# Performance work log

Hardware: AMD Instinct MI355X
Metric: run time of the kernel (lower is better)

The kernel has to match this reference:

```python
import jax, jax.numpy as jnp
import numpy as np
from jax import lax

B, N_ENT, D_ENT = 64, 512, 256
C_SCAT, C_MAP, W = 32, 18, 64
N_RES = 4


def conv2d(x, w, stride, pad):
    return lax.conv_general_dilated(x, w, (stride, stride), [(pad, pad), (pad, pad)],
                                    dimension_numbers=('NCHW', 'OIHW', 'NCHW'))


def batchnorm(x, g, b, eps=1e-5):
    # training-mode BN (batch statistics), matching nn.BatchNorm2d default train()
    mu = x.mean((0, 2, 3), keepdims=True)
    var = x.var((0, 2, 3), keepdims=True)
    return g[None, :, None, None] * (x - mu) * lax.rsqrt(var + eps) + b[None, :, None, None]


def setup_inputs() -> dict:
    key = jax.random.key(0)
    ks = jax.random.split(key, 24)
    s = 0.05
    inp = {
        'x': jax.random.uniform(ks[0], (B, C_MAP, W, W), jnp.float32),
        'entity_embeddings': jax.random.normal(ks[1], (B, N_ENT, D_ENT), jnp.float32),
        'entity_x_y': jax.random.randint(ks[2], (B, N_ENT, 16), 0, 2, jnp.int32),
        'conv1_w': jax.random.normal(ks[3], (C_SCAT, D_ENT), jnp.float32) * s,
        'project_w': jax.random.normal(ks[4], (32, C_SCAT + C_MAP, 1, 1), jnp.float32) * s,
        'project_b': jnp.zeros((32,), jnp.float32),
        'ds1_w': jax.random.normal(ks[5], (64, 32, 4, 4), jnp.float32) * s,
        'ds1_b': jnp.zeros((64,), jnp.float32),
        'ds2_w': jax.random.normal(ks[6], (128, 64, 4, 4), jnp.float32) * s,
        'ds2_b': jnp.zeros((128,), jnp.float32),
        'ds3_w': jax.random.normal(ks[7], (128, 128, 4, 4), jnp.float32) * s,
        'ds3_b': jnp.zeros((128,), jnp.float32),
        'res_conv1_w': jax.random.normal(ks[8], (N_RES, 128, 128, 3, 3), jnp.float32) * s,
        'res_bn1_g': jnp.ones((N_RES, 128), jnp.float32),
        'res_bn1_b': jnp.zeros((N_RES, 128), jnp.float32),
        'res_conv2_w': jax.random.normal(ks[9], (N_RES, 128, 128, 3, 3), jnp.float32) * s,
        'res_bn2_g': jnp.ones((N_RES, 128), jnp.float32),
        'res_bn2_b': jnp.zeros((N_RES, 128), jnp.float32),
        'fc_w': jax.random.normal(ks[10], (256, 8 * 8 * 128), jnp.float32) * s,
        'fc_b': jnp.zeros((256,), jnp.float32),
    }
    return inp


def _scatter(entity_embeddings, entity_x_y, conv1_w):
    # reduced = relu(Conv1d(256->32, k=1)) on entity dim
    reduced = jax.nn.relu(jnp.einsum('bnd,cd->bnc', entity_embeddings, conv1_w))  # [B,N,32]
    bits = entity_x_y
    pow2 = (2 ** jnp.arange(7, -1, -1)).astype(jnp.int32)
    xv = (bits[..., :8] * pow2).sum(-1) // 4   # [B,N] in 0..63
    yv = (bits[..., 8:] * pow2).sum(-1) // 4
    valid = (bits[..., 0] != -1000000000)
    reduced = reduced * valid[..., None].astype(reduced.dtype)
    b_idx = jnp.arange(entity_embeddings.shape[0], dtype=jnp.int32)[:, None]
    flat = (b_idx * (W * W) + yv * W + xv).reshape(-1)
    scat = jax.ops.segment_sum(reduced.reshape(-1, C_SCAT), flat, num_segments=entity_embeddings.shape[0] * W * W)
    return scat.reshape(-1, W, W, C_SCAT).transpose(0, 3, 1, 2)  # [B,32,W,W]


def reference(x, entity_embeddings, entity_x_y, conv1_w, project_w, project_b,
              ds1_w, ds1_b, ds2_w, ds2_b, ds3_w, ds3_b,
              res_conv1_w, res_bn1_g, res_bn1_b, res_conv2_w, res_bn2_g, res_bn2_b,
              fc_w, fc_b):
    scatter_map = _scatter(entity_embeddings, entity_x_y, conv1_w)
    h = jnp.concatenate([scatter_map, x], axis=1)  # [B,50,64,64]
    h = jax.nn.relu(conv2d(h, project_w, 1, 0) + project_b[None, :, None, None])
    h = jax.nn.relu(conv2d(h, ds1_w, 2, 1) + ds1_b[None, :, None, None])   # [B,64,32,32]
    h = jax.nn.relu(conv2d(h, ds2_w, 2, 1) + ds2_b[None, :, None, None])   # [B,128,16,16]
    h = jax.nn.relu(conv2d(h, ds3_w, 2, 1) + ds3_b[None, :, None, None])   # [B,128,8,8]
    map_skip = h
    for i in range(N_RES):
        identity = h
        o = batchnorm(conv2d(h, res_conv1_w[i], 1, 1), res_bn1_g[i], res_bn1_b[i])
        o = jax.nn.relu(o)
        o = batchnorm(conv2d(o, res_conv2_w[i], 1, 1), res_bn2_g[i], res_bn2_b[i])
        h = jax.nn.relu(o + identity)
        map_skip = map_skip + h
    flat = h.reshape(h.shape[0], -1)
    embedded_spatial = jax.nn.relu(flat @ fc_w.T + fc_b)
    return (map_skip, embedded_spatial)
```

## Files before the change

kernel.cpp:

```cpp
#include <hip/hip_runtime.h>
#include <hip/hip_bf16.h>

typedef __attribute__((ext_vector_type(8))) short bf16x8;
typedef __attribute__((ext_vector_type(4))) short bf16x4;
typedef __attribute__((ext_vector_type(4))) float f32x4;

__device__ __forceinline__ short f2bs(float v) {
  __hip_bfloat16 h = __float2bfloat16(v);
  return *reinterpret_cast<short*>(&h);
}

__global__ __launch_bounds__(256) void k_wall(
    const float* __restrict__ rc1w, const float* __restrict__ rc2w,
    const float* __restrict__ d1w, const float* __restrict__ d2w,
    const float* __restrict__ d3w, const float* __restrict__ fcw,
    const float* __restrict__ c1w, const float* __restrict__ pw,
    short* __restrict__ wTr1, short* __restrict__ wTr2, short* __restrict__ wTds1,
    short* __restrict__ wTds2, short* __restrict__ wTds3, short* __restrict__ wfcbf,
    short* __restrict__ wsc, short* __restrict__ wproj,
    float* __restrict__ scat, float* __restrict__ stats) {
  __shared__ float ld[128 * 65];
  const int bx = blockIdx.x;
  const int tid = threadIdx.x;
  if (bx < 8192) {
    ((float4*)scat)[(size_t)bx * 256 + tid] = make_float4(0.f, 0.f, 0.f, 0.f);
  } else if (bx < 12800) {
    const float* src = (bx < 10496) ? rc1w : rc2w;
    short* dst = (bx < 10496) ? wTr1 : wTr2;
    const int i = ((bx - 8192) % 2304) * 256 + tid;
    if (i < 589824) {
      const int layer = i / 147456;
      const int rem = i % 147456;
      const int tap = rem / 16384;
      const int r2 = rem & 16383;
      const int co = r2 >> 7, ci = r2 & 127;
      dst[i] = f2bs(src[(((size_t)layer * 16384 + co * 128 + ci) * 9) + tap]);
    }
  } else if (bx < 14464) {
    int n, base;
    const float* src;
    short* dst;
    if (bx < 12928) { n = 32768; base = 12800; src = d1w; dst = wTds1; }
    else if (bx < 13440) { n = 131072; base = 12928; src = d2w; dst = wTds2; }
    else { n = 262144; base = 13440; src = d3w; dst = wTds3; }
    const int i = (bx - base) * 256 + tid;
    if (i < n) {
      const int COCI = n / 16;
      const int tap = i / COCI;
      const int rem = i % COCI;
      dst[i] = f2bs(src[(size_t)rem * 16 + tap]);
    }
  } else if (bx < 14720) {
    const int j = bx - 14464;
    const float* sp = fcw + (size_t)j * 8192;
    for (int i = tid; i < 8192; i += 256) {
      const int co = i >> 6, pix = i & 63;
      ld[co * 65 + pix] = sp[i];
    }
    __syncthreads();
    short* dp = wfcbf + (size_t)j * 8192;
    for (int i = tid; i < 8192; i += 256) {
      const int pix = i >> 7, co = i & 127;
      dp[i] = f2bs(ld[co * 65 + pix]);
    }
  } else if (bx < 14752) {
    const int i = (bx - 14720) * 256 + tid;
    if (i < 8192) wsc[i] = f2bs(c1w[i]);
  } else if (bx < 14760) {
    const int i = (bx - 14752) * 256 + tid;
    if (i < 2048) {
      const int co = i >> 6, k = i & 63;
      wproj[i] = (k < 50) ? f2bs(pw[co * 50 + k]) : (short)0;
    }
  } else {
    for (int i = tid; i < 2048; i += 256) stats[i] = 0.f;
  }
}

__global__ __launch_bounds__(256) void k_scatmfma(const float* __restrict__ emb,
                                                  const int* __restrict__ xy,
                                                  const short* __restrict__ wsc,
                                                  float* __restrict__ scat_pm) {
  constexpr int CIP = 264;
  __shared__ short abf[64 * CIP];
  __shared__ int flat[64];
  const int tid = threadIdx.x;
  const int e0 = blockIdx.x * 64;
  const float4* eg = (const float4*)(emb + (size_t)e0 * 256);
  for (int i = tid; i < 4096; i += 256) {
    const int e = i >> 6, k4 = i & 63;
    const float4 v = eg[(size_t)e * 64 + k4];
    bf16x4 o;
    o[0] = f2bs(v.x); o[1] = f2bs(v.y); o[2] = f2bs(v.z); o[3] = f2bs(v.w);
    *(bf16x4*)(&abf[e * CIP + k4 * 4]) = o;
  }
  if (tid < 64) {
    const int* bp = xy + (size_t)(e0 + tid) * 16;
    int xv = 0, yv = 0;
#pragma unroll
    for (int j = 0; j < 8; ++j) xv = (xv << 1) | bp[j];
#pragma unroll
    for (int j = 8; j < 16; ++j) yv = (yv << 1) | bp[j];
    flat[tid] = (bp[0] != -1000000000)
                    ? (((e0 + tid) >> 9) * 4096 + ((yv >> 2) << 6) + (xv >> 2))
                    : -1;
  }
  __syncthreads();
  const int wq = __builtin_amdgcn_readfirstlane(tid >> 6);
  const int lane = tid & 63;
  const int l15 = lane & 15, quad = lane >> 4;
  f32x4 acc[2];
  acc[0] = (f32x4){0.f, 0.f, 0.f, 0.f};
  acc[1] = (f32x4){0.f, 0.f, 0.f, 0.f};
  const short* arow = &abf[(wq * 16 + l15) * CIP + quad * 8];
  const short* w0 = wsc + (size_t)l15 * 256 + quad * 8;
  const short* w1 = wsc + (size_t)(16 + l15) * 256 + quad * 8;
#pragma unroll
  for (int kk = 0; kk < 8; ++kk) {
    bf16x8 a = *(const bf16x8*)(arow + kk * 32);
    acc[0] = __builtin_amdgcn_mfma_f32_16x16x32_bf16(a, *(const bf16x8*)(w0 + kk * 32), acc[0], 0, 0, 0);
    acc[1] = __builtin_amdgcn_mfma_f32_16x16x32_bf16(a, *(const bf16x8*)(w1 + kk * 32), acc[1], 0, 0, 0);
  }
#pragma unroll
  for (int nt = 0; nt < 2; ++nt)
#pragma unroll
    for (int r = 0; r < 4; ++r) {
      const int e = wq * 16 + quad * 4 + r;
      const float v = acc[nt][r];
      const int f = flat[e];
      if (f >= 0 && v > 0.f)
        atomicAdd(&scat_pm[(size_t)f * 32 + nt * 16 + l15], v);
    }
}

__global__ __launch_bounds__(256) void k_projmfma(const float* __restrict__ scat_pm,
                                                  const float* __restrict__ xin,
                                                  const short* __restrict__ wproj,
                                                  const float* __restrict__ pb,
                                                  short* __restrict__ h0pm) {
  constexpr int PK = 72;
  __shared__ short abf[128 * PK];
  const int tid = threadIdx.x;
  const int b = blockIdx.x >> 5;
  const int yx0 = (blockIdx.x & 31) << 7;
  const float4* sg = (const float4*)(scat_pm + ((size_t)(b * 4096 + yx0)) * 32);
  for (int i = tid; i < 1024; i += 256) {
    const int p = i >> 3, c4 = i & 7;
    const float4 v = sg[(size_t)p * 8 + c4];
    bf16x4 o;
    o[0] = f2bs(v.x); o[1] = f2bs(v.y); o[2] = f2bs(v.z); o[3] = f2bs(v.w);
    *(bf16x4*)(&abf[p * PK + c4 * 4]) = o;
  }
  for (int i = tid; i < 2304; i += 256) {
    const int run = i >> 7, p = i & 127;
    abf[p * PK + 32 + run] = f2bs(xin[(size_t)(b * 18 + run) * 4096 + yx0 + p]);
  }
  for (int i = tid; i < 2048; i += 256) {
    const int p = i >> 4, k = 50 + (i & 15);
    abf[p * PK + k] = 0;
  }
  __syncthreads();
  const int wq = __builtin_amdgcn_readfirstlane(tid >> 6);
  const int lane = tid & 63;
  const int l15 = lane & 15, quad = lane >> 4;
  f32x4 acc[2][2];
#pragma unroll
  for (int t = 0; t < 2; ++t)
#pragma unroll
    for (int n = 0; n < 2; ++n) acc[t][n] = (f32x4){0.f, 0.f, 0.f, 0.f};
  const short* wb0 = wproj + (size_t)l15 * 64 + quad * 8;
  const short* wb1 = wproj + (size_t)(16 + l15) * 64 + quad * 8;
#pragma unroll
  for (int kk = 0; kk < 2; ++kk) {
    const bf16x8 b0 = *(const bf16x8*)(wb0 + kk * 32);
    const bf16x8 b1 = *(const bf16x8*)(wb1 + kk * 32);
#pragma unroll
    for (int t = 0; t < 2; ++t) {
      const int pix = (wq * 2 + t) * 16 + l15;
      bf16x8 a = *(const bf16x8*)(&abf[pix * PK + quad * 8 + kk * 32]);
      acc[t][0] = __builtin_amdgcn_mfma_f32_16x16x32_bf16(a, b0, acc[t][0], 0, 0, 0);
      acc[t][1] = __builtin_amdgcn_mfma_f32_16x16x32_bf16(a, b1, acc[t][1], 0, 0, 0);
    }
  }
#pragma unroll
  for (int t = 0; t < 2; ++t)
#pragma unroll
    for (int n = 0; n < 2; ++n) {
      const int co = n * 16 + l15;
      const float bv = pb[co];
#pragma unroll
      for (int r = 0; r < 4; ++r) {
        const int pix = (wq * 2 + t) * 16 + quad * 4 + r;
        float v = acc[t][n][r] + bv;
        v = v > 0.f ? v : 0.f;
        h0pm[((size_t)(b * 4096 + yx0 + pix)) * 32 + co] = f2bs(v);
      }
    }
}

template <int CIN, int COUT, int HIN, int ROWSO, int COSPLIT, int MT, int NT, int OUTMODE>
__global__ __launch_bounds__(256) void k_ds2(const short* __restrict__ inpm,
                                             const short* __restrict__ wT,
                                             const float* __restrict__ bias,
                                             short* __restrict__ outbf,
                                             float* __restrict__ outf,
                                             float* __restrict__ msf) {
  constexpr int HOUT = HIN / 2;
  constexpr int ROWS = 2 * ROWSO + 2;
  constexpr int COLS = HIN + 2;
  constexpr int CHUNKS = CIN / 8;
  constexpr int KK = CIN / 32;
  constexpr int CIPAD = CIN + 8;
  constexpr int NHO = HOUT / ROWSO;
  __shared__ short lin[ROWS * COLS * CIPAD];
  const int tid = threadIdx.x;
  int bx = blockIdx.x;
  const int co_blk = (COSPLIT > 1) ? (bx % COSPLIT) : 0;
  if (COSPLIT > 1) bx /= COSPLIT;
  const int hoblk = bx % NHO;
  const int b = bx / NHO;
  for (int i = tid; i < ROWS * COLS * CHUNKS; i += 256) {
    const int ch = i % CHUNKS;
    const int pixv = i / CHUNKS;
    const int r = pixv / COLS, c = pixv % COLS;
    const int hi = 2 * ROWSO * hoblk - 1 + r;
    const int wc = c - 1;
    bf16x8 v = (bf16x8)(short)0;
    if (hi >= 0 && hi < HIN && wc >= 0 && wc < HIN)
      v = *(const bf16x8*)(inpm + ((size_t)(b * HIN + hi) * HIN + wc) * CIN + ch * 8);
    *(bf16x8*)(&lin[(r * COLS + c) * CIPAD + ch * 8]) = v;
  }
  __syncthreads();
  const int wq = __builtin_amdgcn_readfirstlane(tid >> 6);
  const int lane = tid & 63;
  const int l15 = lane & 15, quad = lane >> 4;
  const int mtile = (MT > 1) ? (wq % MT) : 0;
  const int cogrp = wq / MT;
  const int cobase = co_blk * (COUT / COSPLIT) + cogrp * (NT * 16);
  const int p = mtile * 16 + l15;
  const int dr = p / HOUT;
  const int col = p % HOUT;
  f32x4 acc[NT];
#pragma unroll
  for (int n = 0; n < NT; ++n) acc[n] = (f32x4){0.f, 0.f, 0.f, 0.f};
  const short* wrow = wT + (size_t)(cobase + l15) * CIN + quad * 8;
  for (int ky = 0; ky < 4; ++ky) {
    for (int kx = 0; kx < 4; ++kx) {
      const short* arow = &lin[((2 * dr + ky) * COLS + 2 * col + kx) * CIPAD + quad * 8];
      const short* wt = wrow + (size_t)(ky * 4 + kx) * COUT * CIN;
#pragma unroll
      for (int kk = 0; kk < KK; ++kk) {
        bf16x8 a = *(const bf16x8*)(arow + kk * 32);
#pragma unroll
        for (int n = 0; n < NT; ++n) {
          bf16x8 bf = *(const bf16x8*)(wt + n * 16 * CIN + kk * 32);
          acc[n] = __builtin_amdgcn_mfma_f32_16x16x32_bf16(a, bf, acc[n], 0, 0, 0);
        }
      }
    }
  }
#pragma unroll
  for (int n = 0; n < NT; ++n) {
    const int co = cobase + n * 16 + l15;
    const float bv = bias[co];
#pragma unroll
    for (int r = 0; r < 4; ++r) {
      const int pp = mtile * 16 + quad * 4 + r;
      const int dr2 = pp / HOUT;
      const int c2 = pp % HOUT;
      const int ho = hoblk * ROWSO + dr2;
      float v = acc[n][r] + bv;
      v = v > 0.f ? v : 0.f;
      const size_t o = ((size_t)b * HOUT * HOUT + ho * HOUT + c2) * COUT + co;
      outbf[o] = f2bs(v);
      if (OUTMODE == 1) {
        outf[o] = v;
        msf[o] = v;
      }
    }
  }
}

template <int BNIN>
__global__ __launch_bounds__(256) void k_resmfma(const short* __restrict__ hbfin,
                                                 const float* __restrict__ fin,
                                                 const float* __restrict__ statsIn,
                                                 const float* __restrict__ gIn,
                                                 const float* __restrict__ bIn,
                                                 const float* __restrict__ identpm,
                                                 float* __restrict__ houtpm,
                                                 float* __restrict__ mspm,
                                                 const short* __restrict__ wT,
                                                 float* __restrict__ outpm,
                                                 float* __restrict__ statsOut) {
  constexpr int CIPAD = 136;
  __shared__ short lin[100 * CIPAD];
  __shared__ float bnsc[128], bnsh[128];
  const int tid = threadIdx.x;
  const int b = blockIdx.x >> 3;
  const int cobase = (blockIdx.x & 7) << 4;
  if (BNIN >= 1) {
    if (tid < 128) {
      const float mu = statsIn[tid] * (1.f / 4096.f);
      const float var = statsIn[128 + tid] * (1.f / 4096.f) - mu * mu;
      const float sc = gIn[tid] * rsqrtf(var + 1e-5f);
      bnsc[tid] = sc;
      bnsh[tid] = bIn[tid] - mu * sc;
    }
    __syncthreads();
  }
  if (BNIN == 0) {
    const short* hb = hbfin + ((size_t)b << 13);
    for (int i = tid; i < 1600; i += 256) {
      const int pixel = i >> 4, ch = i & 15;
      const int r = pixel / 10, c = pixel % 10;
      bf16x8 v = (bf16x8)(short)0;
      if (r >= 1 && r <= 8 && c >= 1 && c <= 8)
        v = *(const bf16x8*)(hb + (((r - 1) << 3) + (c - 1)) * 128 + ch * 8);
      *(bf16x8*)(&lin[pixel * CIPAD + ch * 8]) = v;
    }
  } else if (BNIN == 1) {
    const float* fb = fin + ((size_t)b << 13);
    for (int i = tid; i < 3200; i += 256) {
      const int pixel = i >> 5, c4 = i & 31;
      const int r = pixel / 10, c = pixel % 10;
      bf16x4 o = (bf16x4)(short)0;
      if (r >= 1 && r <= 8 && c >= 1 && c <= 8) {
        const float4 x = *(const float4*)(fb + (size_t)(((r - 1) << 3) + (c - 1)) * 128 + c4 * 4);
        const float xv[4] = {x.x, x.y, x.z, x.w};
#pragma unroll
        for (int k = 0; k < 4; ++k) {
          const int ci = c4 * 4 + k;
          const float v = xv[k] * bnsc[ci] + bnsh[ci];
          o[k] = f2bs(v > 0.f ? v : 0.f);
        }
      }
      *(bf16x4*)(&lin[pixel * CIPAD + c4 * 4]) = o;
    }
  } else {
    const float* fb = fin + ((size_t)b << 13);
    const float* ib = identpm + ((size_t)b << 13);
    float* hb = houtpm + ((size_t)b << 13);
    float* mb = mspm + ((size_t)b << 13);
    const bool wr = (cobase == 0);
    for (int i = tid; i < 3200; i += 256) {
      const int pixel = i >> 5, c4 = i & 31;
      const int r = pixel / 10, c = pixel % 10;
      bf16x4 o = (bf16x4)(short)0;
      if (r >= 1 && r <= 8 && c >= 1 && c <= 8) {
        const size_t gi = (size_t)(((r - 1) << 3) + (c - 1)) * 128 + c4 * 4;
        const float4 x = *(const float4*)(fb + gi);
        const float4 idv = *(const float4*)(ib + gi);
        const float xv[4] = {x.x, x.y, x.z, x.w};
        const float iv[4] = {idv.x, idv.y, idv.z, idv.w};
        float vv[4];
#pragma unroll
        for (int k = 0; k < 4; ++k) {
          const int ci = c4 * 4 + k;
          float v = xv[k] * bnsc[ci] + bnsh[ci] + iv[k];
          v = v > 0.f ? v : 0.f;
          vv[k] = v;
          o[k] = f2bs(v);
        }
        if (wr) {
          *(float4*)(hb + gi) = make_float4(vv[0], vv[1], vv[2], vv[3]);
          const float4 m = *(const float4*)(mb + gi);
          *(float4*)(mb + gi) = make_float4(m.x + vv[0], m.y + vv[1], m.z + vv[2], m.w + vv[3]);
        }
      }
      *(bf16x4*)(&lin[pixel * CIPAD + c4 * 4]) = o;
    }
  }
  __syncthreads();
  const int wq = __builtin_amdgcn_readfirstlane(tid >> 6);
  const int lane = tid & 63;
  const int l15 = lane & 15, quad = lane >> 4;
  const int p = wq * 16 + l15;
  const int py = p >> 3, px = p & 7;
  f32x4 acc = (f32x4){0.f, 0.f, 0.f, 0.f};
  const short* wrow = wT + (size_t)(cobase + l15) * 128 + quad * 8;
  for (int t = 0; t < 9; ++t) {
    const int ky = t / 3, kx = t % 3;
    const short* arow = &lin[((py + ky) * 10 + px + kx) * CIPAD + quad * 8];
    const short* wt = wrow + (size_t)t * 16384;
#pragma unroll
    for (int kk = 0; kk < 4; ++kk) {
      bf16x8 a = *(const bf16x8*)(arow + kk * 32);
      bf16x8 bf = *(const bf16x8*)(wt + kk * 32);
      acc = __builtin_amdgcn_mfma_f32_16x16x32_bf16(a, bf, acc, 0, 0, 0);
    }
  }
  float* ob = outpm + ((size_t)b << 13);
  const int co = cobase + l15;
  float s = 0.f, q = 0.f;
#pragma unroll
  for (int r = 0; r < 4; ++r) {
    const float v = acc[r];
    ob[(size_t)(wq * 16 + quad * 4 + r) * 128 + co] = v;
    s += v;
    q += v * v;
  }
  s += __shfl_down(s, 32); q += __shfl_down(q, 32);
  s += __shfl_down(s, 16); q += __shfl_down(q, 16);
  if (lane < 16) {
    atomicAdd(&statsOut[co], s);
    atomicAdd(&statsOut[128 + co], q);
  }
}

__global__ __launch_bounds__(256) void k_bnfinal(const float* __restrict__ tmp2pm,
                                                 const float* __restrict__ stats,
                                                 const float* __restrict__ g,
                                                 const float* __restrict__ bb,
                                                 const float* __restrict__ identpm,
                                                 const float* __restrict__ mspm,
                                                 float* __restrict__ out0,
                                                 short* __restrict__ hbf) {
  __shared__ float t[64 * 132];
  __shared__ float bnsc[128], bnsh[128];
  const int b = blockIdx.x;
  const int tid = threadIdx.x;
  if (tid < 128) {
    const float mu = stats[tid] * (1.f / 4096.f);
    const float var = stats[128 + tid] * (1.f / 4096.f) - mu * mu;
    const float sc = g[tid] * rsqrtf(var + 1e-5f);
    bnsc[tid] = sc;
    bnsh[tid] = bb[tid] - mu * sc;
  }
  __syncthreads();
  const size_t base = (size_t)b << 13;
  for (int i = tid; i < 8192; i += 256) {
    const int co = i & 127, pix = i >> 7;
    float v = tmp2pm[base + i] * bnsc[co] + bnsh[co] + identpm[base + i];
    v = v > 0.f ? v : 0.f;
    hbf[base + i] = f2bs(v);
    t[pix * 132 + co] = mspm[base + i] + v;
  }
  __syncthreads();
  float* dp = out0 + base;
  for (int i = tid; i < 8192; i += 256) {
    const int co = i >> 6, pix = i & 63;
    dp[i] = t[pix * 132 + co];
  }
}

__global__ __launch_bounds__(256) void k_fcmfma(const short* __restrict__ hbf,
                                                const short* __restrict__ wbf,
                                                float* __restrict__ part) {
  const int nb = blockIdx.x & 3;
  const int kb = blockIdx.x >> 2;
  const int wq = __builtin_amdgcn_readfirstlane((int)(threadIdx.x >> 6));
  const int lane = threadIdx.x & 63;
  const int l15 = lane & 15, quad = lane >> 4;
  const int k0 = kb * 256 + quad * 8;
  const short* wp = wbf + (size_t)(nb * 64 + wq * 16 + l15) * 8192 + k0;
  const short* hp = hbf + (size_t)l15 * 8192 + k0;
  f32x4 acc[4];
#pragma unroll
  for (int m = 0; m < 4; ++m) acc[m] = (f32x4){0.f, 0.f, 0.f, 0.f};
  for (int ks = 0; ks < 8; ++ks) {
    bf16x8 bfr = *(const bf16x8*)(wp + ks * 32);
#pragma unroll
    for (int m = 0; m < 4; ++m) {
      bf16x8 a = *(const bf16x8*)(hp + (size_t)m * 16 * 8192 + ks * 32);
      acc[m] = __builtin_amdgcn_mfma_f32_16x16x32_bf16(a, bfr, acc[m], 0, 0, 0);
    }
  }
#pragma unroll
  for (int m = 0; m < 4; ++m)
#pragma unroll
    for (int r = 0; r < 4; ++r) {
      const int b = m * 16 + quad * 4 + r;
      part[((size_t)kb * 64 + b) * 256 + nb * 64 + wq * 16 + l15] = acc[m][r];
    }
}

__global__ __launch_bounds__(256) void k_fcred(const float* __restrict__ part,
                                               const float* __restrict__ bias,
                                               float* __restrict__ out1) {
  const int idx = blockIdx.x * 256 + threadIdx.x;
  const int j = idx & 255;
  float s = 0.f;
#pragma unroll 8
  for (int kb = 0; kb < 32; ++kb) s += part[(size_t)kb * 16384 + idx];
  const float v = s + bias[j];
  out1[idx] = v > 0.f ? v : 0.f;
}

extern "C" void kernel_launch(void* const* d_in, const int* in_sizes, int n_in,
                              void* d_out, int out_size, void* d_ws, size_t ws_size,
                              hipStream_t stream) {
  const float* xin = (const float*)d_in[0];
  const float* emb = (const float*)d_in[1];
  const int* xy = (const int*)d_in[2];
  const float* c1w = (const float*)d_in[3];
  const float* pw = (const float*)d_in[4];
  const float* pb = (const float*)d_in[5];
  const float* d1w = (const float*)d_in[6];
  const float* d1b = (const float*)d_in[7];
  const float* d2w = (const float*)d_in[8];
  const float* d2b = (const float*)d_in[9];
  const float* d3w = (const float*)d_in[10];
  const float* d3b = (const float*)d_in[11];
  const float* rc1w = (const float*)d_in[12];
  const float* rbn1g = (const float*)d_in[13];
  const float* rbn1b = (const float*)d_in[14];
  const float* rc2w = (const float*)d_in[15];
  const float* rbn2g = (const float*)d_in[16];
  const float* rbn2b = (const float*)d_in[17];
  const float* fcw = (const float*)d_in[18];
  const float* fcb = (const float*)d_in[19];

  float* out0 = (float*)d_out;
  float* out1 = out0 + 524288;

  float* F = (float*)d_ws;
  float* scat = F + 0;
  float* h1pm_f = F + 0;
  float* h2pm_f = F + 2097152;
  float* hApm = F + 3145728;
  float* hBpm = F + 3670016;
  float* tmppm = F + 4194304;
  float* tmp2pm = F + 4718592;
  float* mspm = F + 5242880;
  short* pmbfA = (short*)(F + 5767168);
  short* hfinbf = (short*)(F + 6029312);
  float* stats = F + 6291456;
  float* fcpart = F + 6293504;
  short* h0pm = (short*)(F + 8388608);
  short* wfcbf = (short*)(F + 12582912);
  short* wTr1 = (short*)(F + 13631488);
  short* wTr2 = wTr1 + 589824;
  short* wTds1 = wTr2 + 589824;
  short* wTds2 = wTds1 + 32768;
  short* wTds3 = wTds2 + 131072;
  short* wsc = wTds3 + 262144;
  short* wproj = wsc + 8192;

  k_wall<<<14761, 256, 0, stream>>>(rc1w, rc2w, d1w, d2w, d3w, fcw, c1w, pw,
                                    wTr1, wTr2, wTds1, wTds2, wTds3, wfcbf, wsc, wproj,
                                    scat, stats);
  k_scatmfma<<<512, 256, 0, stream>>>(emb, xy, wsc, scat);
  k_projmfma<<<2048, 256, 0, stream>>>(scat, xin, wproj, pb, h0pm);
  short* h1pm = (short*)h1pm_f;
  short* h2pm = (short*)h2pm_f;
  k_ds2<32, 64, 64, 2, 1, 4, 4, 0><<<1024, 256, 0, stream>>>(h0pm, wTds1, d1b, h1pm, hApm, mspm);
  k_ds2<64, 128, 32, 1, 1, 1, 2, 0><<<1024, 256, 0, stream>>>(h1pm, wTds2, d2b, h2pm, hApm, mspm);
  k_ds2<128, 128, 16, 2, 2, 1, 1, 1><<<512, 256, 0, stream>>>(h2pm, wTds3, d3b, pmbfA, hApm, mspm);

  float* ident = hApm;
  float* identN = hBpm;
  for (int i = 0; i < 4; ++i) {
    float* sA = stats + i * 512;
    float* sB = stats + i * 512 + 256;
    if (i == 0) {
      k_resmfma<0><<<512, 256, 0, stream>>>(pmbfA, nullptr, nullptr, nullptr, nullptr,
                                            nullptr, nullptr, nullptr,
                                            wTr1, tmppm, sA);
    } else {
      float* sBp = stats + (i - 1) * 512 + 256;
      k_resmfma<2><<<512, 256, 0, stream>>>(nullptr, tmp2pm, sBp, rbn2g + (i - 1) * 128,
                                            rbn2b + (i - 1) * 128, ident, identN, mspm,
                                            wTr1 + (size_t)i * 147456, tmppm, sA);
      float* sw = ident; ident = identN; identN = sw;
    }
    k_resmfma<1><<<512, 256, 0, stream>>>(nullptr, tmppm, sA, rbn1g + i * 128, rbn1b + i * 128,
                                          nullptr, nullptr, nullptr,
                                          wTr2 + (size_t)i * 147456, tmp2pm, sB);
  }
  k_bnfinal<<<64, 256, 0, stream>>>(tmp2pm, stats + 3 * 512 + 256, rbn2g + 384, rbn2b + 384,
                                    ident, mspm, out0, hfinbf);
  k_fcmfma<<<128, 256, 0, stream>>>(hfinbf, wfcbf, fcpart);
  k_fcred<<<64, 256, 0, stream>>>(fcpart, fcb, out1);
}
```

Before: 412.2 us.

## Fuse residual chain into one persistent kernel with software grid barriers

Replaces the eight residual conv launches and the final BN kernel with one persistent kernel of 512 blocks. Stages are separated by an atomic-counter grid barrier instead of kernel boundaries, and the final BN/output step is spread across all blocks. This removes roughly eight launch gaps and the tail drain between stages. In exchange it depends on all 512 blocks being co-resident (launch bounds set to 2 blocks per CU) and adds spin-wait barrier overhead.

```diff
diff --git a/kernel.cpp b/kernel.cpp
--- a/kernel.cpp
+++ b/kernel.cpp
@@ -18,7 +18,7 @@
     short* __restrict__ wTr1, short* __restrict__ wTr2, short* __restrict__ wTds1,
     short* __restrict__ wTds2, short* __restrict__ wTds3, short* __restrict__ wfcbf,
     short* __restrict__ wsc, short* __restrict__ wproj,
-    float* __restrict__ scat, float* __restrict__ stats) {
+    float* __restrict__ scat, float* __restrict__ stats, int* __restrict__ bar) {
   __shared__ float ld[128 * 65];
   const int bx = blockIdx.x;
   const int tid = threadIdx.x;
@@ -74,6 +74,7 @@
     }
   } else {
     for (int i = tid; i < 2048; i += 256) stats[i] = 0.f;
+    if (tid == 0) bar[0] = 0;
   }
 }
 
@@ -281,25 +282,31 @@
   }
 }
 
-template <int BNIN>
-__global__ __launch_bounds__(256) void k_resmfma(const short* __restrict__ hbfin,
-                                                 const float* __restrict__ fin,
-                                                 const float* __restrict__ statsIn,
-                                                 const float* __restrict__ gIn,
-                                                 const float* __restrict__ bIn,
-                                                 const float* __restrict__ identpm,
-                                                 float* __restrict__ houtpm,
-                                                 float* __restrict__ mspm,
-                                                 const short* __restrict__ wT,
-                                                 float* __restrict__ outpm,
-                                                 float* __restrict__ statsOut) {
+__device__ __forceinline__ void gridbar(int* __restrict__ bar, int phase) {
+  __syncthreads();
+  if (threadIdx.x == 0) {
+    __threadfence();
+    __hip_atomic_fetch_add(bar, 1, __ATOMIC_ACQ_REL, __HIP_MEMORY_SCOPE_AGENT);
+    while (__hip_atomic_load(bar, __ATOMIC_ACQUIRE, __HIP_MEMORY_SCOPE_AGENT) < 512 * phase) {
+      __builtin_amdgcn_s_sleep(2);
+    }
+  }
+  __syncthreads();
+}
+
+template <int MODE>
+__device__ __forceinline__ void res_stage(
+    const short* __restrict__ hbfin, const float* __restrict__ fin,
+    const float* __restrict__ statsIn, const float* __restrict__ gIn,
+    const float* __restrict__ bIn, const float* __restrict__ identpm,
+    float* __restrict__ houtpm, float* __restrict__ mspm,
+    const short* __restrict__ wT, float* __restrict__ outpm,
+    float* __restrict__ statsOut, short* lin, float* bnsc, float* bnsh) {
   constexpr int CIPAD = 136;
-  __shared__ short lin[100 * CIPAD];
-  __shared__ float bnsc[128], bnsh[128];
   const int tid = threadIdx.x;
   const int b = blockIdx.x >> 3;
   const int cobase = (blockIdx.x & 7) << 4;
-  if (BNIN >= 1) {
+  if (MODE >= 1) {
     if (tid < 128) {
       const float mu = statsIn[tid] * (1.f / 4096.f);
       const float var = statsIn[128 + tid] * (1.f / 4096.f) - mu * mu;
@@ -309,7 +316,7 @@
     }
     __syncthreads();
   }
-  if (BNIN == 0) {
+  if (MODE == 0) {
     const short* hb = hbfin + ((size_t)b << 13);
     for (int i = tid; i < 1600; i += 256) {
       const int pixel = i >> 4, ch = i & 15;
@@ -319,7 +326,7 @@
         v = *(const bf16x8*)(hb + (((r - 1) << 3) + (c - 1)) * 128 + ch * 8);
       *(bf16x8*)(&lin[pixel * CIPAD + ch * 8]) = v;
     }
-  } else if (BNIN == 1) {
+  } else if (MODE == 1) {
     const float* fb = fin + ((size_t)b << 13);
     for (int i = tid; i < 3200; i += 256) {
       const int pixel = i >> 5, c4 = i & 31;
@@ -408,39 +415,64 @@
   }
 }
 
-__global__ __launch_bounds__(256) void k_bnfinal(const float* __restrict__ tmp2pm,
-                                                 const float* __restrict__ stats,
-                                                 const float* __restrict__ g,
-                                                 const float* __restrict__ bb,
-                                                 const float* __restrict__ identpm,
-                                                 const float* __restrict__ mspm,
-                                                 float* __restrict__ out0,
-                                                 short* __restrict__ hbf) {
-  __shared__ float t[64 * 132];
+__global__ __launch_bounds__(256, 2) void k_reschain(
+    const short* __restrict__ h0bf, float* __restrict__ tmppm, float* __restrict__ tmp2pm,
+    float* __restrict__ hA, float* __restrict__ hB, float* __restrict__ mspm,
+    const float* __restrict__ rbn1g, const float* __restrict__ rbn1b,
+    const float* __restrict__ rbn2g, const float* __restrict__ rbn2b,
+    const short* __restrict__ wTr1, const short* __restrict__ wTr2,
+    float* __restrict__ stats, int* __restrict__ bar,
+    float* __restrict__ out0, short* __restrict__ hfinbf) {
+  __shared__ short lin[100 * 136];
   __shared__ float bnsc[128], bnsh[128];
-  const int b = blockIdx.x;
+  __shared__ float tfin[64 * 17];
+  int phase = 0;
+  float* ident = hA;
+  float* identN = hB;
+  for (int i = 0; i < 4; ++i) {
+    float* sA = stats + i * 512;
+    float* sB = sA + 256;
+    if (i == 0) {
+      res_stage<0>(h0bf, nullptr, nullptr, nullptr, nullptr, nullptr, nullptr, nullptr,
+                   wTr1, tmppm, sA, lin, bnsc, bnsh);
+    } else {
+      const float* sBp = stats + (i - 1) * 512 + 256;
+      res_stage<2>(nullptr, tmp2pm, sBp, rbn2g + (i - 1) * 128, rbn2b + (i - 1) * 128,
+                   ident, identN, mspm, wTr1 + (size_t)i * 147456, tmppm, sA, lin, bnsc, bnsh);
+      float* t = ident; ident = identN; identN = t;
+    }
+    gridbar(bar, ++phase);
+    res_stage<1>(nullptr, tmppm, sA, rbn1g + i * 128, rbn1b + i * 128, nullptr, nullptr,
+                 nullptr, wTr2 + (size_t)i * 147456, tmp2pm, sB, lin, bnsc, bnsh);
+    gridbar(bar, ++phase);
+  }
   const int tid = threadIdx.x;
   if (tid < 128) {
-    const float mu = stats[tid] * (1.f / 4096.f);
-    const float var = stats[128 + tid] * (1.f / 4096.f) - mu * mu;
-    const float sc = g[tid] * rsqrtf(var + 1e-5f);
+    const float* s3 = stats + 3 * 512 + 256;
+    const float mu = s3[tid] * (1.f / 4096.f);
+    const float var = s3[128 + tid] * (1.f / 4096.f) - mu * mu;
+    const float sc = rbn2g[384 + tid] * rsqrtf(var + 1e-5f);
     bnsc[tid] = sc;
-    bnsh[tid] = bb[tid] - mu * sc;
-  }
-  __syncthreads();
+    bnsh[tid] = rbn2b[384 + tid] - mu * sc;
+  }
+  __syncthreads();
+  const int b = blockIdx.x >> 3;
+  const int co0 = (blockIdx.x & 7) << 4;
   const size_t base = (size_t)b << 13;
-  for (int i = tid; i < 8192; i += 256) {
-    const int co = i & 127, pix = i >> 7;
-    float v = tmp2pm[base + i] * bnsc[co] + bnsh[co] + identpm[base + i];
+  for (int i = tid; i < 1024; i += 256) {
+    const int pix = i >> 4, c = i & 15;
+    const int co = co0 + c;
+    const size_t gi = base + (size_t)pix * 128 + co;
+    float v = tmp2pm[gi] * bnsc[co] + bnsh[co] + ident[gi];
     v = v > 0.f ? v : 0.f;
-    hbf[base + i] = f2bs(v);
-    t[pix * 132 + co] = mspm[base + i] + v;
+    hfinbf[gi] = f2bs(v);
+    tfin[pix * 17 + c] = mspm[gi] + v;
   }
   __syncthreads();
   float* dp = out0 + base;
-  for (int i = tid; i < 8192; i += 256) {
-    const int co = i >> 6, pix = i & 63;
-    dp[i] = t[pix * 132 + co];
+  for (int i = tid; i < 1024; i += 256) {
+    const int c = i >> 6, pix = i & 63;
+    dp[(size_t)(co0 + c) * 64 + pix] = tfin[pix * 17 + c];
   }
 }
 
@@ -526,7 +558,8 @@
   short* pmbfA = (short*)(F + 5767168);
   short* hfinbf = (short*)(F + 6029312);
   float* stats = F + 6291456;
-  float* fcpart = F + 6293504;
+  int* bar = (int*)(F + 6293504);
+  float* fcpart = F + 6293568;
   short* h0pm = (short*)(F + 8388608);
   short* wfcbf = (short*)(F + 12582912);
   short* wTr1 = (short*)(F + 13631488);
@@ -539,7 +572,7 @@
 
   k_wall<<<14761, 256, 0, stream>>>(rc1w, rc2w, d1w, d2w, d3w, fcw, c1w, pw,
                                     wTr1, wTr2, wTds1, wTds2, wTds3, wfcbf, wsc, wproj,
-                                    scat, stats);
+                                    scat, stats, bar);
   k_scatmfma<<<512, 256, 0, stream>>>(emb, xy, wsc, scat);
   k_projmfma<<<2048, 256, 0, stream>>>(scat, xin, wproj, pb, h0pm);
   short* h1pm = (short*)h1pm_f;
@@ -548,28 +581,9 @@
   k_ds2<64, 128, 32, 1, 1, 1, 2, 0><<<1024, 256, 0, stream>>>(h1pm, wTds2, d2b, h2pm, hApm, mspm);
   k_ds2<128, 128, 16, 2, 2, 1, 1, 1><<<512, 256, 0, stream>>>(h2pm, wTds3, d3b, pmbfA, hApm, mspm);
 
-  float* ident = hApm;
-  float* identN = hBpm;
-  for (int i = 0; i < 4; ++i) {
-    float* sA = stats + i * 512;
-    float* sB = stats + i * 512 + 256;
-    if (i == 0) {
-      k_resmfma<0><<<512, 256, 0, stream>>>(pmbfA, nullptr, nullptr, nullptr, nullptr,
-                                            nullptr, nullptr, nullptr,
-                                            wTr1, tmppm, sA);
-    } else {
-      float* sBp = stats + (i - 1) * 512 + 256;
-      k_resmfma<2><<<512, 256, 0, stream>>>(nullptr, tmp2pm, sBp, rbn2g + (i - 1) * 128,
-                                            rbn2b + (i - 1) * 128, ident, identN, mspm,
-                                            wTr1 + (size_t)i * 147456, tmppm, sA);
-      float* sw = ident; ident = identN; identN = sw;
-    }
-    k_resmfma<1><<<512, 256, 0, stream>>>(nullptr, tmppm, sA, rbn1g + i * 128, rbn1b + i * 128,
-                                          nullptr, nullptr, nullptr,
-                                          wTr2 + (size_t)i * 147456, tmp2pm, sB);
-  }
-  k_bnfinal<<<64, 256, 0, stream>>>(tmp2pm, stats + 3 * 512 + 256, rbn2g + 384, rbn2b + 384,
-                                    ident, mspm, out0, hfinbf);
+  k_reschain<<<512, 256, 0, stream>>>(pmbfA, tmppm, tmp2pm, hApm, hBpm, mspm,
+                                      rbn1g, rbn1b, rbn2g, rbn2b, wTr1, wTr2,
+                                      stats, bar, out0, hfinbf);
   k_fcmfma<<<128, 256, 0, stream>>>(hfinbf, wfcbf, fcpart);
   k_fcred<<<64, 256, 0, stream>>>(fcpart, fcb, out1);
 }
```

Measured after the change: 726.0 us. 76.1% more time.
